# Performance work log

Measured on AMD Instinct MI355X. Metric: run time of the kernel, lower is better.

## Reference

```python
import jax, jax.numpy as jnp
import numpy as np

MAX_CLUSTERS = 5
CLUSTER_SIZE_MAX = 3
K_HOP = 2
TAU = 1.0  # epoch=0 -> tau_init * decay^0 = 1.0
NEG = -1e9


def _logits(x, ctx, W1, b1, W2, b2):
    # x: [B,N,D], ctx: [B,H] -> logits [B,N] (selection_mlp, dropout=eval/identity)
    B, N, _ = x.shape
    h = jnp.concatenate([x, jnp.broadcast_to(ctx[:, None, :], (B, N, ctx.shape[-1]))], axis=-1)
    h = jax.nn.relu(h @ W1.T + b1)
    return (h @ W2.T + b2)[..., 0]


def _select(logits, cand, key):
    # Hard Gumbel-Softmax argmax over candidate nodes; zeros row if no candidates.
    any_c = cand.any(axis=-1, keepdims=True)
    ml = jnp.where(cand, logits, NEG)
    u = jax.random.uniform(key, logits.shape, dtype=logits.dtype)
    g = -jnp.log(-jnp.log(u + 1e-8) + 1e-8)
    idx = jnp.argmax((ml + g) / TAU, axis=-1)
    oh = jax.nn.one_hot(idx, logits.shape[-1], dtype=logits.dtype)
    return oh * any_c.astype(logits.dtype)


def _gru(seq, h0, Wih, Whh, bih, bhh):
    # torch nn.GRU single layer, batch_first; seq: [B,T,D], h0: [B,H] -> final hidden [B,H]
    def cell(h, xt):
        gi = xt @ Wih.T + bih
        gh = h @ Whh.T + bhh
        ir, iz, inn = jnp.split(gi, 3, axis=-1)
        hr, hz, hn = jnp.split(gh, 3, axis=-1)
        r = jax.nn.sigmoid(ir + hr)
        z = jax.nn.sigmoid(iz + hz)
        n = jnp.tanh(inn + r * hn)
        return (1.0 - z) * n + z * h, None
    h, _ = jax.lax.scan(cell, h0, jnp.swapaxes(seq, 0, 1))
    return h


def reference(x, adj, mask, W1, b1, W2, b2, Wc, bc, Wih, Whh, bih, bhh):
    B, N, D = x.shape
    key = jax.random.key(42)
    avail = mask.astype(bool)
    ctx = x.mean(axis=1) @ Wc.T + bc          # context_init  [B,H]
    h_gru = jnp.zeros_like(ctx)               # context_hidden
    assign = jnp.zeros((B, N, MAX_CLUSTERS), x.dtype)
    embs, hist = [], []
    for c in range(MAX_CLUSTERS):
        # logits are identical for every selection within this cluster (same x, same context)
        logits = _logits(x, ctx, W1, b1, W2, b2)  # [B,N]
        # seed selection (torch uses .item() -> selection is a constant index; no grad path)
        seed = jax.lax.stop_gradient(_select(logits, avail, jax.random.fold_in(key, 2 * c)))
        avail = avail & ~(seed > 0.5)
        # k-hop BFS from seed via adjacency matvecs
        reach = seed > 0.5
        cur = seed
        for _ in range(K_HOP):
            nb = jnp.einsum('bn,bnm->bm', cur, adj) > 0
            new = nb & ~reach
            reach = reach | nb
            cur = new.astype(x.dtype)
        member = seed
        for a in range(CLUSTER_SIZE_MAX - 1):
            cand = avail & reach
            sel = jax.lax.stop_gradient(_select(logits, cand, jax.random.fold_in(key, 2 * c + 1000 + a)))
            avail = avail & ~(sel > 0.5)
            member = member + sel
        assign = assign.at[:, :, c].set(member)
        cnt = member.sum(axis=-1, keepdims=True)
        emb = jnp.einsum('bn,bnd->bd', member, x) / jnp.maximum(cnt, 1.0)  # mean of member feats; 0 if empty
        embs.append(emb)
        hist.append(emb)
        # torch re-runs the GRU over the FULL cluster history each iteration, starting
        # from the previously updated hidden state (faithful to the original code)
        h_gru = _gru(jnp.stack(hist, axis=1), h_gru, Wih, Whh, bih, bhh)
        ctx = h_gru
    cluster_features = jnp.stack(embs, axis=1)               # [B,S,D]
    S = MAX_CLUSTERS
    cluster_adj = jnp.ones((B, S, S), x.dtype) - jnp.eye(S, dtype=x.dtype)[None]
    return cluster_features, cluster_adj, assign


def setup_inputs() -> dict:
    key = jax.random.key(0)
    ks = jax.random.split(key, 10)
    B, N, D, H = 16, 2048, 128, 64
    x = jax.random.normal(ks[0], (B, N, D), dtype=jnp.float32)
    # sparse symmetric binary adjacency, ~16 neighbors per node
    a = (jax.random.uniform(ks[1], (B, N, N)) < 0.004).astype(jnp.float32)
    adj = jnp.clip(a + jnp.swapaxes(a, 1, 2), 0.0, 1.0)
    adj = adj * (1.0 - jnp.eye(N, dtype=jnp.float32)[None])
    mask = jnp.ones((B, N), dtype=jnp.int32)
    s = 0.05
    return {
        'x': x, 'adj': adj, 'mask': mask,
        'W1': jax.random.normal(ks[2], (H, D + H)) * s, 'b1': jnp.zeros((H,)),
        'W2': jax.random.normal(ks[3], (1, H)) * s, 'b2': jnp.zeros((1,)),
        'Wc': jax.random.normal(ks[4], (H, D)) * s, 'bc': jnp.zeros((H,)),
        'Wih': jax.random.normal(ks[5], (3 * H, D)) * s,
        'Whh': jax.random.normal(ks[6], (3 * H, H)) * s,
        'bih': jnp.zeros((3 * H,)), 'bhh': jnp.zeros((3 * H,)),
    }
```

## Files before the change

kernel.cpp:

```cpp
#include <hip/hip_runtime.h>
#include <cfloat>
#include <cmath>

#define NB 2048
#define BB 16
#define DD 128
#define HH 64
#define MAXC 5
#define CSMAX 3
#define NT 1024

__device__ __forceinline__ unsigned rotl32(unsigned v, int d) {
  return (v << d) | (v >> (32 - d));
}

__device__ __forceinline__ void tf2x32(unsigned k0, unsigned k1, unsigned x0, unsigned x1,
                                       unsigned& o0, unsigned& o1) {
  unsigned ks2 = k0 ^ k1 ^ 0x1BD11BDAu;
  x0 += k0; x1 += k1;
#define RND(r) { x0 += x1; x1 = rotl32(x1, r); x1 ^= x0; }
  RND(13) RND(15) RND(26) RND(6)   x0 += k1;  x1 += ks2 + 1u;
  RND(17) RND(29) RND(16) RND(24)  x0 += ks2; x1 += k0 + 2u;
  RND(13) RND(15) RND(26) RND(6)   x0 += k0;  x1 += k1 + 3u;
  RND(17) RND(29) RND(16) RND(24)  x0 += k1;  x1 += ks2 + 4u;
  RND(13) RND(15) RND(26) RND(6)   x0 += ks2; x1 += k0 + 5u;
#undef RND
  o0 = x0; o1 = x1;
}

__device__ __forceinline__ float gumbel_for(unsigned k0, unsigned k1, unsigned idx) {
  unsigned o0, o1;
  tf2x32(k0, k1, 0u, idx, o0, o1);
  unsigned bits = o0 ^ o1;
  float u = __uint_as_float((bits >> 9) | 0x3f800000u) - 1.0f;
  float uu = u + 1e-8f;
  return -logf(-logf(uu) + 1e-8f);
}

__global__ __launch_bounds__(NT) void gvp_prep(
    const float* __restrict__ x, const float* __restrict__ W1,
    float* __restrict__ P, float* __restrict__ partial, float* __restrict__ gumb) {
  __shared__ __align__(16) float s_W1[HH][DD + 4];
  __shared__ float sp[8][DD];
  const int bid = blockIdx.x, tid = threadIdx.x;

  if (bid < 128) {
    for (int i = tid; i < HH * (DD / 4); i += NT) {
      int r = i >> 5, q = i & 31;
      *(float4*)&s_W1[r][q * 4] = *(const float4*)(W1 + (size_t)r * (DD + HH) + q * 4);
    }
    __syncthreads();
    const int jg = tid & 15, ng = tid >> 4;
    const int j0 = jg * 4;
    const size_t n0 = (size_t)bid * 256 + ng * 4;
    const float4* x4 = (const float4*)x;
    float acc[4][4];
#pragma unroll
    for (int i = 0; i < 4; i++)
#pragma unroll
      for (int q = 0; q < 4; q++) acc[i][q] = 0.f;
    for (int kq = 0; kq < 32; kq++) {
      float4 xv[4], wv[4];
#pragma unroll
      for (int i = 0; i < 4; i++) xv[i] = x4[(n0 + i) * 32 + kq];
#pragma unroll
      for (int q = 0; q < 4; q++) wv[q] = *(const float4*)&s_W1[j0 + q][kq * 4];
#pragma unroll
      for (int i = 0; i < 4; i++)
#pragma unroll
        for (int q = 0; q < 4; q++)
          acc[i][q] += xv[i].x * wv[q].x + xv[i].y * wv[q].y +
                       xv[i].z * wv[q].z + xv[i].w * wv[q].w;
    }
#pragma unroll
    for (int i = 0; i < 4; i++)
#pragma unroll
      for (int q = 0; q < 4; q++)
        P[(n0 + i) * HH + j0 + q] = acc[i][q];
  } else if (bid < 384) {
    const int bm = bid - 128;
    const int b = bm >> 4, chunk = bm & 15;
    const int d = tid & (DD - 1), part = tid >> 7;
    float acc = 0.f;
    const int base = chunk * 128 + part;
#pragma unroll
    for (int k = 0; k < 16; k++)
      acc += x[((size_t)b * NB + base + k * 8) * DD + d];
    sp[part][d] = acc;
    __syncthreads();
    if (tid < DD) {
      float m = 0.f;
#pragma unroll
      for (int p = 0; p < 8; p++) m += sp[p][tid];
      partial[((size_t)b * 16 + chunk) * DD + tid] = m;
    }
  } else {
    const int bg = bid - 384;
    const int base = (bg * NT + tid) * 4;
#pragma unroll
    for (int i = 0; i < 4; i++) {
      int idx = base + i;
      int sel = idx >> 15;
      int rem = idx & 32767;
      int c = sel / 3, s = sel - 3 * c;
      unsigned data = (s == 0) ? (unsigned)(2 * c) : (unsigned)(2 * c + 1000 + (s - 1));
      unsigned k0, k1;
      tf2x32(0u, 42u, 0u, data, k0, k1);
      gumb[idx] = gumbel_for(k0, k1, (unsigned)rem);
    }
  }
}

__global__ __launch_bounds__(NT, 4) void gvp_main(
    const float* __restrict__ x, const float* __restrict__ adj, const int* __restrict__ mask,
    const float* __restrict__ W1, const float* __restrict__ b1,
    const float* __restrict__ W2, const float* __restrict__ b2,
    const float* __restrict__ Wc, const float* __restrict__ bc,
    const float* __restrict__ Wih, const float* __restrict__ Whh,
    const float* __restrict__ bih, const float* __restrict__ bhh,
    const float* __restrict__ P, const float* __restrict__ partial,
    const float* __restrict__ gumb,
    float* __restrict__ out_feat, float* __restrict__ out_adjm, float* __restrict__ out_assign) {
  const int b = blockIdx.x;
  const int tid = threadIdx.x;

  __shared__ __align__(16) float s_logits[NB];
  __shared__ __align__(16) float s_gumb[2][NB];
  __shared__ unsigned char s_avail[NB], s_reach[NB], s_assignB[NB];
  __shared__ short s_list[128];
  __shared__ int s_cnt;
  __shared__ unsigned long long s_key[CSMAX];
  __shared__ __align__(16) float s_ctx[HH], s_q[HH];
  __shared__ __align__(16) float s_h[2][HH];
  __shared__ __align__(16) float s_hist[MAXC][DD];
  __shared__ __align__(16) float s_giAll[MAXC][3 * HH];
  __shared__ __align__(16) float s_Whh[3 * HH][HH + 4];
  __shared__ __align__(16) float s_W1c[HH][HH + 4];
  __shared__ __align__(16) float s_W2[HH];
  __shared__ float s_bhh[3 * HH], s_b1[HH];
  __shared__ __align__(16) float s_mean[DD];
  __shared__ float s_b2v;

  const size_t xb = (size_t)b * NB * DD;
  const float4* adj4 = (const float4*)(adj + (size_t)b * NB * NB);
  const float4* P4 = (const float4*)(P + (size_t)b * NB * HH);

  auto scanReduce = [&](float bv, int bi, int slot) {
#pragma unroll
    for (int off = 32; off; off >>= 1) {
      float ov = __shfl_down(bv, off);
      int oi = __shfl_down(bi, off);
      if (ov > bv || (ov == bv && oi < bi)) { bv = ov; bi = oi; }
    }
    if ((tid & 63) == 0 && bi < NB) {
      unsigned u = __float_as_uint(bv);
      u = (u & 0x80000000u) ? ~u : (u | 0x80000000u);
      unsigned long long key = ((unsigned long long)u << 32) | (unsigned)(~bi);
      atomicMax(&s_key[slot], key);
    }
  };
  auto decodeIdx = [](unsigned long long k) -> int {
    return k ? (int)(unsigned)(~(unsigned)k) : -1;
  };

  for (int i = tid; i < 3 * HH * (HH / 4); i += NT) {
    int r = i >> 4, q = i & 15;
    *(float4*)&s_Whh[r][q * 4] = *(const float4*)(Whh + (size_t)r * HH + q * 4);
  }
  {
    int r = tid >> 4, q = tid & 15;
    *(float4*)&s_W1c[r][q * 4] = *(const float4*)(W1 + (size_t)r * (DD + HH) + DD + q * 4);
  }
  if (tid < 3 * HH) s_bhh[tid] = bhh[tid];
  if (tid < HH) { s_W2[tid] = W2[tid]; s_b1[tid] = b1[tid]; s_h[0][tid] = 0.f; }
  if (tid == 0) s_b2v = b2[0];
#pragma unroll
  for (int r = 0; r < 2; r++) {
    int n = tid + r * NT;
    s_avail[n] = (mask[b * NB + n] != 0) ? 1 : 0;
    s_assignB[n] = 0;
  }
  if (tid < DD) {
    float m = 0.f;
#pragma unroll
    for (int k = 0; k < 16; k++) m += partial[((size_t)b * 16 + k) * DD + tid];
    s_mean[tid] = m * (1.0f / NB);
  }
  __syncthreads();
  if (tid < 4 * HH) {
    int row = tid >> 2, g = tid & 3;
    const float4* wr = (const float4*)(Wc + (size_t)row * DD) + g * 8;
    const float4* m4 = (const float4*)s_mean + g * 8;
    float s = 0.f;
#pragma unroll
    for (int i = 0; i < 8; i++) {
      float4 w = wr[i], m = m4[i];
      s += w.x * m.x + w.y * m.y + w.z * m.z + w.w * m.w;
    }
    s += __shfl_xor(s, 1);
    s += __shfl_xor(s, 2);
    if (g == 0) s_ctx[row] = s + bc[row];
  }
  __syncthreads();

  int hp = 0;

  for (int c = 0; c < MAXC; c++) {
    const float* g0p = gumb + ((size_t)(c * 3) * BB + b) * NB;
    const float4* g12 = (const float4*)(gumb + ((size_t)(c * 3 + 1 + (tid >> 9)) * BB + b) * NB);
    float4 gst = g12[tid & 511];
    const int n0 = tid, n1 = tid + NT;
    float gs0 = g0p[n0], gs1 = g0p[n1];
    ((float4*)s_gumb)[tid] = gst;
    if (tid < 4 * HH) {
      int row = tid >> 2, g = tid & 3;
      const float4* wr = (const float4*)&s_W1c[row][0] + g * 4;
      const float4* c4 = (const float4*)s_ctx + g * 4;
      float s = 0.f;
#pragma unroll
      for (int i = 0; i < 4; i++) {
        float4 w = wr[i], cc = c4[i];
        s += w.x * cc.x + w.y * cc.y + w.z * cc.z + w.w * cc.w;
      }
      s += __shfl_xor(s, 1);
      s += __shfl_xor(s, 2);
      if (g == 0) s_q[row] = s + s_b1[row];
    }
    if (tid < CSMAX) s_key[tid] = 0ull;
    if (tid == 0) s_cnt = 0;
    __syncthreads();

    {
      float l0 = s_b2v, l1 = s_b2v;
      const float4* p0 = P4 + (size_t)n0 * 16;
      const float4* p1 = P4 + (size_t)n1 * 16;
      const float4* q4 = (const float4*)s_q;
      const float4* w4 = (const float4*)s_W2;
#pragma unroll
      for (int qq = 0; qq < 16; qq += 4) {
        float4 A[4], Bv[4];
#pragma unroll
        for (int i = 0; i < 4; i++) { A[i] = p0[qq + i]; Bv[i] = p1[qq + i]; }
#pragma unroll
        for (int i = 0; i < 4; i++) {
          float4 qv = q4[qq + i], w = w4[qq + i];
          l0 += w.x * fmaxf(A[i].x + qv.x, 0.f) + w.y * fmaxf(A[i].y + qv.y, 0.f) +
                w.z * fmaxf(A[i].z + qv.z, 0.f) + w.w * fmaxf(A[i].w + qv.w, 0.f);
          l1 += w.x * fmaxf(Bv[i].x + qv.x, 0.f) + w.y * fmaxf(Bv[i].y + qv.y, 0.f) +
                w.z * fmaxf(Bv[i].z + qv.z, 0.f) + w.w * fmaxf(Bv[i].w + qv.w, 0.f);
        }
      }
      s_logits[n0] = l0;
      s_logits[n1] = l1;
      float bv = -FLT_MAX;
      int bi = NB;
      if (s_avail[n0]) { float y = l0 + gs0; if (y > bv) { bv = y; bi = n0; } }
      if (s_avail[n1]) { float y = l1 + gs1; if (y > bv || (y == bv && n1 < bi)) { bv = y; bi = n1; } }
      scanReduce(bv, bi, 0);
    }
    __syncthreads();

    const int seed = decodeIdx(s_key[0]);
    if (tid < 512) {
      if (seed >= 0) {
        float4 a = adj4[(size_t)seed * 512 + tid];
        int m = tid << 2;
        unsigned f0 = a.x > 0.f, f1 = a.y > 0.f, f2 = a.z > 0.f, f3 = a.w > 0.f;
        unsigned r = f0 | (f1 << 8) | (f2 << 16) | (f3 << 24);
        if ((seed >> 2) == tid) r |= 1u << ((seed & 3) * 8);
        ((unsigned*)s_reach)[tid] = r;
        if (f0 && m != seed)     { int p = atomicAdd(&s_cnt, 1); if (p < 128) s_list[p] = (short)m; }
        if (f1 && m + 1 != seed) { int p = atomicAdd(&s_cnt, 1); if (p < 128) s_list[p] = (short)(m + 1); }
        if (f2 && m + 2 != seed) { int p = atomicAdd(&s_cnt, 1); if (p < 128) s_list[p] = (short)(m + 2); }
        if (f3 && m + 3 != seed) { int p = atomicAdd(&s_cnt, 1); if (p < 128) s_list[p] = (short)(m + 3); }
      } else {
        ((unsigned*)s_reach)[tid] = 0u;
      }
    }
    __syncthreads();

    if (seed >= 0) {
      int cnt = min(s_cnt, 128);
      int m4 = tid & 511, rg = tid >> 9;
      bool a0 = false, a1 = false, a2 = false, a3 = false;
#pragma unroll
      for (int k = 0; k < 20; k++) {
        int li = rg + 2 * k;
        if (li < cnt) {
          int n = s_list[li];
          float4 a = adj4[(size_t)n * 512 + m4];
          a0 |= a.x > 0.f; a1 |= a.y > 0.f; a2 |= a.z > 0.f; a3 |= a.w > 0.f;
        }
      }
      for (int li = rg + 40; li < cnt; li += 2) {
        int n = s_list[li];
        float4 a = adj4[(size_t)n * 512 + m4];
        a0 |= a.x > 0.f; a1 |= a.y > 0.f; a2 |= a.z > 0.f; a3 |= a.w > 0.f;
      }
      int m = m4 << 2;
      if (a0) s_reach[m] = 1;
      if (a1) s_reach[m + 1] = 1;
      if (a2) s_reach[m + 2] = 1;
      if (a3) s_reach[m + 3] = 1;
    }
    __syncthreads();

    {
      float bv = -FLT_MAX;
      int bi = NB;
#pragma unroll
      for (int r = 0; r < 2; r++) {
        int n = tid + r * NT;
        if (s_avail[n] && s_reach[n] && n != seed) {
          float y = s_logits[n] + s_gumb[0][n];
          if (y > bv || (y == bv && n < bi)) { bv = y; bi = n; }
        }
      }
      scanReduce(bv, bi, 1);
    }
    __syncthreads();

    const int w1i = decodeIdx(s_key[1]);
    {
      float bv = -FLT_MAX;
      int bi = NB;
#pragma unroll
      for (int r = 0; r < 2; r++) {
        int n = tid + r * NT;
        if (s_avail[n] && s_reach[n] && n != seed && n != w1i) {
          float y = s_logits[n] + s_gumb[1][n];
          if (y > bv || (y == bv && n < bi)) { bv = y; bi = n; }
        }
      }
      scanReduce(bv, bi, 2);
    }
    __syncthreads();

    const int w2i = decodeIdx(s_key[2]);
    {
      int mc = (seed >= 0) + (w1i >= 0) + (w2i >= 0);
      if (tid < DD) {
        float acc = 0.f;
        if (seed >= 0) acc += x[xb + (size_t)seed * DD + tid];
        if (w1i >= 0) acc += x[xb + (size_t)w1i * DD + tid];
        if (w2i >= 0) acc += x[xb + (size_t)w2i * DD + tid];
        float e = acc / fmaxf((float)mc, 1.0f);
        s_hist[c][tid] = e;
        out_feat[((size_t)b * MAXC + c) * DD + tid] = e;
      } else if (tid >= 128 && tid < 128 + CSMAX) {
        int idx = (tid == 128) ? seed : (tid == 129 ? w1i : w2i);
        if (idx >= 0) { s_avail[idx] = 0; s_assignB[idx] |= (unsigned char)(1 << c); }
      }
    }
    __syncthreads();

    if (tid < 4 * 3 * HH) {
      int row = tid >> 2, g = tid & 3;
      const float4* wr = (const float4*)(Wih + (size_t)row * DD) + g * 8;
      const float4* h4 = (const float4*)s_hist[c] + g * 8;
      float s = 0.f;
#pragma unroll
      for (int i = 0; i < 8; i++) {
        float4 w = wr[i], hh = h4[i];
        s += w.x * hh.x + w.y * hh.y + w.z * hh.z + w.w * hh.w;
      }
      s += __shfl_xor(s, 1);
      s += __shfl_xor(s, 2);
      if (g == 0) s_giAll[c][row] = s + bih[row];
    }
    __syncthreads();

    for (int t0 = 0; t0 <= c; t0++) {
      if (tid < 4 * HH) {
        int row = tid >> 2, g = tid & 3;
        const float4* h4 = (const float4*)s_h[hp] + g * 4;
        float4 hv[4];
#pragma unroll
        for (int i = 0; i < 4; i++) hv[i] = h4[i];
        const float4* wr = (const float4*)&s_Whh[row][0] + g * 4;
        const float4* wz = (const float4*)&s_Whh[HH + row][0] + g * 4;
        const float4* wn = (const float4*)&s_Whh[2 * HH + row][0] + g * 4;
        float sr = 0.f, sz = 0.f, sn = 0.f;
#pragma unroll
        for (int i = 0; i < 4; i++) {
          float4 a = wr[i], bz = wz[i], cn = wn[i], h = hv[i];
          sr += a.x * h.x + a.y * h.y + a.z * h.z + a.w * h.w;
          sz += bz.x * h.x + bz.y * h.y + bz.z * h.z + bz.w * h.w;
          sn += cn.x * h.x + cn.y * h.y + cn.z * h.z + cn.w * h.w;
        }
        sr += __shfl_xor(sr, 1); sr += __shfl_xor(sr, 2);
        sz += __shfl_xor(sz, 1); sz += __shfl_xor(sz, 2);
        sn += __shfl_xor(sn, 1); sn += __shfl_xor(sn, 2);
        if (g == 0) {
          float r = 1.f / (1.f + expf(-(s_giAll[t0][row] + sr + s_bhh[row])));
          float z = 1.f / (1.f + expf(-(s_giAll[t0][HH + row] + sz + s_bhh[HH + row])));
          float nn = tanhf(s_giAll[t0][2 * HH + row] + r * (sn + s_bhh[2 * HH + row]));
          float hn = (1.f - z) * nn + z * s_h[hp][row];
          s_h[hp ^ 1][row] = hn;
          if (t0 == c) s_ctx[row] = hn;
        }
      }
      hp ^= 1;
      __syncthreads();
    }
  }

#pragma unroll
  for (int r = 0; r < 2; r++) {
    int n = tid + r * NT;
    unsigned bits = s_assignB[n];
    size_t base = ((size_t)(b * NB + n)) * MAXC;
#pragma unroll
    for (int cc = 0; cc < MAXC; cc++)
      out_assign[base + cc] = (float)((bits >> cc) & 1u);
  }
  for (int i = tid; i < MAXC * MAXC; i += NT)
    out_adjm[(size_t)b * MAXC * MAXC + i] = ((i / MAXC) == (i % MAXC)) ? 0.f : 1.f;
}

extern "C" void kernel_launch(void* const* d_in, const int* in_sizes, int n_in,
                              void* d_out, int out_size, void* d_ws, size_t ws_size,
                              hipStream_t stream) {
  const float* x   = (const float*)d_in[0];
  const float* adj = (const float*)d_in[1];
  const int*   mask= (const int*)d_in[2];
  const float* W1  = (const float*)d_in[3];
  const float* b1  = (const float*)d_in[4];
  const float* W2  = (const float*)d_in[5];
  const float* b2  = (const float*)d_in[6];
  const float* Wc  = (const float*)d_in[7];
  const float* bc  = (const float*)d_in[8];
  const float* Wih = (const float*)d_in[9];
  const float* Whh = (const float*)d_in[10];
  const float* bih = (const float*)d_in[11];
  const float* bhh = (const float*)d_in[12];

  float* ws = (float*)d_ws;
  float* P       = ws;
  float* partial = P + (size_t)BB * NB * HH;
  float* gumb    = partial + (size_t)BB * 16 * DD;

  float* out = (float*)d_out;
  float* out_feat = out;
  float* out_adjm = out + (size_t)BB * MAXC * DD;
  float* out_assign = out_adjm + (size_t)BB * MAXC * MAXC;

  hipLaunchKernelGGL(gvp_prep, dim3(504), dim3(NT), 0, stream, x, W1, P, partial, gumb);
  hipLaunchKernelGGL(gvp_main, dim3(BB), dim3(NT), 0, stream,
                     x, adj, mask, W1, b1, W2, b2, Wc, bc, Wih, Whh, bih, bhh, P, partial, gumb,
                     out_feat, out_adjm, out_assign);
}
```

Baseline: 195.0 us.

## Overlap GRU replay steps with other phases and prefetch P rows and Gumbel noise

The first one or two GRU replay steps of each cluster now run on otherwise idle thread ranges during the embedding and Wih-projection phases, which removes some serial barrier-separated steps. Each thread's first P row is held in registers across all clusters, and the next cluster's Gumbel noise is prefetched early to hide global load latency. The cost is much higher register pressure from the 16 cached float4 values, which may reduce occupancy or cause spills. Bookkeeping threads also move to different ranges so they do not collide with the new GRU work.

After: 209.3 us. 1.07x slower.

```diff
diff --git a/kernel.cpp b/kernel.cpp
--- a/kernel.cpp
+++ b/kernel.cpp
@@ -144,6 +144,7 @@
   const size_t xb = (size_t)b * NB * DD;
   const float4* adj4 = (const float4*)(adj + (size_t)b * NB * NB);
   const float4* P4 = (const float4*)(P + (size_t)b * NB * HH);
+  const int n0 = tid, n1 = tid + NT;
 
   auto scanReduce = [&](float bv, int bi, int slot) {
 #pragma unroll
@@ -163,6 +164,12 @@
     return k ? (int)(unsigned)(~(unsigned)k) : -1;
   };
 
+  float4 pP[16];
+  {
+    const float4* pr0 = P4 + (size_t)n0 * 16;
+#pragma unroll
+    for (int i = 0; i < 16; i++) pP[i] = pr0[i];
+  }
   for (int i = tid; i < 3 * HH * (HH / 4); i += NT) {
     int r = i >> 4, q = i & 15;
     *(float4*)&s_Whh[r][q * 4] = *(const float4*)(Whh + (size_t)r * HH + q * 4);
@@ -185,6 +192,14 @@
 #pragma unroll
     for (int k = 0; k < 16; k++) m += partial[((size_t)b * 16 + k) * DD + tid];
     s_mean[tid] = m * (1.0f / NB);
+  }
+  float4 gst;
+  float g0a, g0b;
+  {
+    const float* g0p = gumb + ((size_t)0 * BB + b) * NB;
+    g0a = g0p[n0]; g0b = g0p[n1];
+    const float4* g12 = (const float4*)(gumb + ((size_t)(1 + (tid >> 9)) * BB + b) * NB);
+    gst = g12[tid & 511];
   }
   __syncthreads();
   if (tid < 4 * HH) {
@@ -205,12 +220,40 @@
 
   int hp = 0;
 
+  auto gruStep = [&](int t, int lo, int c) {
+    int tt = tid - lo;
+    if ((unsigned)tt < 256u) {
+      int row = tt >> 2, g = tt & 3;
+      const float4* h4 = (const float4*)s_h[hp] + g * 4;
+      float4 hv[4];
+#pragma unroll
+      for (int i = 0; i < 4; i++) hv[i] = h4[i];
+      const float4* wr = (const float4*)&s_Whh[row][0] + g * 4;
+      const float4* wz = (const float4*)&s_Whh[HH + row][0] + g * 4;
+      const float4* wn = (const float4*)&s_Whh[2 * HH + row][0] + g * 4;
+      float sr = 0.f, sz = 0.f, sn = 0.f;
+#pragma unroll
+      for (int i = 0; i < 4; i++) {
+        float4 a = wr[i], bz = wz[i], cn = wn[i], h = hv[i];
+        sr += a.x * h.x + a.y * h.y + a.z * h.z + a.w * h.w;
+        sz += bz.x * h.x + bz.y * h.y + bz.z * h.z + bz.w * h.w;
+        sn += cn.x * h.x + cn.y * h.y + cn.z * h.z + cn.w * h.w;
+      }
+      sr += __shfl_xor(sr, 1); sr += __shfl_xor(sr, 2);
+      sz += __shfl_xor(sz, 1); sz += __shfl_xor(sz, 2);
+      sn += __shfl_xor(sn, 1); sn += __shfl_xor(sn, 2);
+      if (g == 0) {
+        float r = 1.f / (1.f + expf(-(s_giAll[t][row] + sr + s_bhh[row])));
+        float z = 1.f / (1.f + expf(-(s_giAll[t][HH + row] + sz + s_bhh[HH + row])));
+        float nn = tanhf(s_giAll[t][2 * HH + row] + r * (sn + s_bhh[2 * HH + row]));
+        float hn = (1.f - z) * nn + z * s_h[hp][row];
+        s_h[hp ^ 1][row] = hn;
+        if (t == c) s_ctx[row] = hn;
+      }
+    }
+  };
+
   for (int c = 0; c < MAXC; c++) {
-    const float* g0p = gumb + ((size_t)(c * 3) * BB + b) * NB;
-    const float4* g12 = (const float4*)(gumb + ((size_t)(c * 3 + 1 + (tid >> 9)) * BB + b) * NB);
-    float4 gst = g12[tid & 511];
-    const int n0 = tid, n1 = tid + NT;
-    float gs0 = g0p[n0], gs1 = g0p[n1];
     ((float4*)s_gumb)[tid] = gst;
     if (tid < 4 * HH) {
       int row = tid >> 2, g = tid & 3;
@@ -226,36 +269,44 @@
       s += __shfl_xor(s, 2);
       if (g == 0) s_q[row] = s + s_b1[row];
     }
-    if (tid < CSMAX) s_key[tid] = 0ull;
-    if (tid == 0) s_cnt = 0;
+    if (tid >= 512 && tid < 512 + CSMAX) s_key[tid - 512] = 0ull;
+    if (tid == 768) s_cnt = 0;
     __syncthreads();
 
     {
-      float l0 = s_b2v, l1 = s_b2v;
-      const float4* p0 = P4 + (size_t)n0 * 16;
       const float4* p1 = P4 + (size_t)n1 * 16;
       const float4* q4 = (const float4*)s_q;
       const float4* w4 = (const float4*)s_W2;
-#pragma unroll
-      for (int qq = 0; qq < 16; qq += 4) {
-        float4 A[4], Bv[4];
-#pragma unroll
-        for (int i = 0; i < 4; i++) { A[i] = p0[qq + i]; Bv[i] = p1[qq + i]; }
-#pragma unroll
-        for (int i = 0; i < 4; i++) {
-          float4 qv = q4[qq + i], w = w4[qq + i];
-          l0 += w.x * fmaxf(A[i].x + qv.x, 0.f) + w.y * fmaxf(A[i].y + qv.y, 0.f) +
-                w.z * fmaxf(A[i].z + qv.z, 0.f) + w.w * fmaxf(A[i].w + qv.w, 0.f);
-          l1 += w.x * fmaxf(Bv[i].x + qv.x, 0.f) + w.y * fmaxf(Bv[i].y + qv.y, 0.f) +
-                w.z * fmaxf(Bv[i].z + qv.z, 0.f) + w.w * fmaxf(Bv[i].w + qv.w, 0.f);
-        }
+      float4 Pa[8];
+#pragma unroll
+      for (int i = 0; i < 8; i++) Pa[i] = p1[i];
+      float l0 = s_b2v, l1 = s_b2v;
+#pragma unroll
+      for (int i = 0; i < 16; i++) {
+        float4 p = pP[i], qv = q4[i], w = w4[i];
+        l0 += w.x * fmaxf(p.x + qv.x, 0.f) + w.y * fmaxf(p.y + qv.y, 0.f) +
+              w.z * fmaxf(p.z + qv.z, 0.f) + w.w * fmaxf(p.w + qv.w, 0.f);
+      }
+#pragma unroll
+      for (int i = 0; i < 8; i++) {
+        float4 p = Pa[i], qv = q4[i], w = w4[i];
+        l1 += w.x * fmaxf(p.x + qv.x, 0.f) + w.y * fmaxf(p.y + qv.y, 0.f) +
+              w.z * fmaxf(p.z + qv.z, 0.f) + w.w * fmaxf(p.w + qv.w, 0.f);
+      }
+#pragma unroll
+      for (int i = 0; i < 8; i++) Pa[i] = p1[8 + i];
+#pragma unroll
+      for (int i = 0; i < 8; i++) {
+        float4 p = Pa[i], qv = q4[8 + i], w = w4[8 + i];
+        l1 += w.x * fmaxf(p.x + qv.x, 0.f) + w.y * fmaxf(p.y + qv.y, 0.f) +
+              w.z * fmaxf(p.z + qv.z, 0.f) + w.w * fmaxf(p.w + qv.w, 0.f);
       }
       s_logits[n0] = l0;
       s_logits[n1] = l1;
       float bv = -FLT_MAX;
       int bi = NB;
-      if (s_avail[n0]) { float y = l0 + gs0; if (y > bv) { bv = y; bi = n0; } }
-      if (s_avail[n1]) { float y = l1 + gs1; if (y > bv || (y == bv && n1 < bi)) { bv = y; bi = n1; } }
+      if (s_avail[n0]) { float y = l0 + g0a; if (y > bv) { bv = y; bi = n0; } }
+      if (s_avail[n1]) { float y = l1 + g0b; if (y > bv || (y == bv && n1 < bi)) { bv = y; bi = n1; } }
       scanReduce(bv, bi, 0);
     }
     __syncthreads();
@@ -337,6 +388,13 @@
     __syncthreads();
 
     const int w2i = decodeIdx(s_key[2]);
+    if (c + 1 < MAXC) {
+      const float* g0p = gumb + ((size_t)((c + 1) * 3) * BB + b) * NB;
+      g0a = g0p[n0]; g0b = g0p[n1];
+      const float4* g12 =
+          (const float4*)(gumb + ((size_t)((c + 1) * 3 + 1 + (tid >> 9)) * BB + b) * NB);
+      gst = g12[tid & 511];
+    }
     {
       int mc = (seed >= 0) + (w1i >= 0) + (w2i >= 0);
       if (tid < DD) {
@@ -347,12 +405,14 @@
         float e = acc / fmaxf((float)mc, 1.0f);
         s_hist[c][tid] = e;
         out_feat[((size_t)b * MAXC + c) * DD + tid] = e;
-      } else if (tid >= 128 && tid < 128 + CSMAX) {
-        int idx = (tid == 128) ? seed : (tid == 129 ? w1i : w2i);
+      } else if (tid >= 512 && tid < 512 + CSMAX) {
+        int idx = (tid == 512) ? seed : (tid == 513 ? w1i : w2i);
         if (idx >= 0) { s_avail[idx] = 0; s_assignB[idx] |= (unsigned char)(1 << c); }
       }
-    }
-    __syncthreads();
+      if (c >= 1) gruStep(0, 256, c);
+    }
+    __syncthreads();
+    if (c >= 1) hp ^= 1;
 
     if (tid < 4 * 3 * HH) {
       int row = tid >> 2, g = tid & 3;
@@ -368,38 +428,13 @@
       s += __shfl_xor(s, 2);
       if (g == 0) s_giAll[c][row] = s + bih[row];
     }
-    __syncthreads();
-
-    for (int t0 = 0; t0 <= c; t0++) {
-      if (tid < 4 * HH) {
-        int row = tid >> 2, g = tid & 3;
-        const float4* h4 = (const float4*)s_h[hp] + g * 4;
-        float4 hv[4];
-#pragma unroll
-        for (int i = 0; i < 4; i++) hv[i] = h4[i];
-        const float4* wr = (const float4*)&s_Whh[row][0] + g * 4;
-        const float4* wz = (const float4*)&s_Whh[HH + row][0] + g * 4;
-        const float4* wn = (const float4*)&s_Whh[2 * HH + row][0] + g * 4;
-        float sr = 0.f, sz = 0.f, sn = 0.f;
-#pragma unroll
-        for (int i = 0; i < 4; i++) {
-          float4 a = wr[i], bz = wz[i], cn = wn[i], h = hv[i];
-          sr += a.x * h.x + a.y * h.y + a.z * h.z + a.w * h.w;
-          sz += bz.x * h.x + bz.y * h.y + bz.z * h.z + bz.w * h.w;
-          sn += cn.x * h.x + cn.y * h.y + cn.z * h.z + cn.w * h.w;
-        }
-        sr += __shfl_xor(sr, 1); sr += __shfl_xor(sr, 2);
-        sz += __shfl_xor(sz, 1); sz += __shfl_xor(sz, 2);
-        sn += __shfl_xor(sn, 1); sn += __shfl_xor(sn, 2);
-        if (g == 0) {
-          float r = 1.f / (1.f + expf(-(s_giAll[t0][row] + sr + s_bhh[row])));
-          float z = 1.f / (1.f + expf(-(s_giAll[t0][HH + row] + sz + s_bhh[HH + row])));
-          float nn = tanhf(s_giAll[t0][2 * HH + row] + r * (sn + s_bhh[2 * HH + row]));
-          float hn = (1.f - z) * nn + z * s_h[hp][row];
-          s_h[hp ^ 1][row] = hn;
-          if (t0 == c) s_ctx[row] = hn;
-        }
-      }
+    if (c >= 2) gruStep(1, 768, c);
+    __syncthreads();
+    if (c >= 2) hp ^= 1;
+
+    int t0 = (c == 0) ? 0 : (c == 1) ? 1 : 2;
+    for (int t = t0; t <= c; t++) {
+      gruStep(t, 0, c);
       hp ^= 1;
       __syncthreads();
     }
```
